# Kernel tuning notes

Measured on AMD Instinct MI355X. Metric: run time of the kernel, lower is better.

The kernel has to match this reference:

```python
import jax, jax.numpy as jnp
import numpy as np
import math

S, B, D, H = 2048, 4, 1024, 16
DH = D // H

def setup_inputs() -> dict:
    key = jax.random.key(0)
    ks = jax.random.split(key, 6)
    x = jax.random.normal(ks[0], (S, B, D), dtype=jnp.float32)
    # causal additive mask (finite large negative for numerical safety)
    i = jnp.arange(S)
    attn_mask = jnp.where(i[None, :] > i[:, None], jnp.float32(-1e9), jnp.float32(0.0))
    beta = jnp.zeros((H,), dtype=jnp.float32)  # per-head log-scale, init 0 -> exp=1
    xav = math.sqrt(6.0 / (D + D))  # xavier_uniform bound
    Wq = jax.random.uniform(ks[1], (D, D), minval=-xav, maxval=xav, dtype=jnp.float32)
    Wk = jax.random.uniform(ks[2], (D, D), minval=-xav, maxval=xav, dtype=jnp.float32)
    Wv = jax.random.uniform(ks[3], (D, D), minval=-xav, maxval=xav, dtype=jnp.float32)
    Wo = jax.random.uniform(ks[4], (D, D), minval=-xav, maxval=xav, dtype=jnp.float32)
    z = jnp.zeros((D,), dtype=jnp.float32)
    return {"x": x, "attn_mask": attn_mask, "beta": beta,
            "Wq": Wq, "bq": z, "Wk": Wk, "bk": z, "Wv": Wv, "bv": z, "Wo": Wo, "bo": z}

def reference(x, attn_mask, beta, Wq, bq, Wk, bk, Wv, bv, Wo, bo):
    s, b, d = x.shape
    h, dh = H, DH
    q = x @ Wq.T + bq  # (s, b, d)
    k = x @ Wk.T + bk
    v = x @ Wv.T + bv
    # attn_sink: append zero key/value token, pad mask with a zero column
    k = jnp.concatenate([k, jnp.zeros((1, b, d), k.dtype)], axis=0)  # (s+1, b, d)
    v = jnp.concatenate([v, jnp.zeros((1, b, d), v.dtype)], axis=0)
    mask = jnp.pad(attn_mask, ((0, 0), (0, 1)))  # (s, s+1)
    t = s + 1
    # split heads: (seq, b, h, dh) -> (b, h, seq, dh)
    qh = q.reshape(s, b, h, dh).transpose(1, 2, 0, 3)
    kh = k.reshape(t, b, h, dh).transpose(1, 2, 0, 3)
    vh = v.reshape(t, b, h, dh).transpose(1, 2, 0, 3)
    scale = (jnp.exp(beta) * math.sqrt(dh))[None, :, None, None]
    qh = qh / scale
    scores = jnp.einsum('bhsd,bhtd->bhst', qh, kh) + mask[None, None]
    w = jax.nn.softmax(scores, axis=-1)
    out = jnp.einsum('bhst,bhtd->bhsd', w, vh)  # (b, h, s, dh)
    out = out.transpose(2, 0, 1, 3).reshape(s, b, d)
    return out @ Wo.T + bo
```

## Files before the change

### kernel.cpp

```cpp
#include <hip/hip_runtime.h>
#include <hip/hip_bf16.h>
#include <math.h>

#define S_LEN   2048
#define BATCH   4
#define DMODEL  1024
#define NHEAD   16
#define DHEAD   64
#define MROWS   (S_LEN * BATCH)

typedef __bf16 bf16;
typedef __bf16 bf16x8 __attribute__((ext_vector_type(8)));
typedef __bf16 bf16x4 __attribute__((ext_vector_type(4)));
typedef short  short4_t __attribute__((ext_vector_type(4)));
typedef float  f32x4  __attribute__((ext_vector_type(4)));

#define LOG2E 1.4426950408889634f

#define AS1C(p) (const __attribute__((address_space(1))) void*)(p)
#define AS3(p)  (__attribute__((address_space(3))) void*)(p)


__global__ __launch_bounds__(256) void cast_bf16(const float* __restrict__ in,
                                                 bf16* __restrict__ out, int n8) {
    int i = blockIdx.x * 256 + threadIdx.x;
    if (i >= n8) return;
    const float4* p = (const float4*)in;
    float4 a = p[i * 2], b = p[i * 2 + 1];
    bf16x8 o;
    o[0] = (bf16)a.x; o[1] = (bf16)a.y; o[2] = (bf16)a.z; o[3] = (bf16)a.w;
    o[4] = (bf16)b.x; o[5] = (bf16)b.y; o[6] = (bf16)b.z; o[7] = (bf16)b.w;
    *(bf16x8*)(out + (size_t)i * 8) = o;
}

__global__ __launch_bounds__(256) void cast3_bf16(const float* __restrict__ w0,
                                                  const float* __restrict__ w1,
                                                  const float* __restrict__ w2,
                                                  bf16* __restrict__ out) {
    const int seg = blockIdx.y;
    const float* in = (seg == 0) ? w0 : (seg == 1) ? w1 : w2;
    int i = blockIdx.x * 256 + threadIdx.x;
    const float4* p = (const float4*)in;
    float4 a = p[i * 2], b = p[i * 2 + 1];
    bf16x8 o;
    o[0] = (bf16)a.x; o[1] = (bf16)a.y; o[2] = (bf16)a.z; o[3] = (bf16)a.w;
    o[4] = (bf16)b.x; o[5] = (bf16)b.y; o[6] = (bf16)b.z; o[7] = (bf16)b.w;
    *(bf16x8*)(out + (size_t)seg * DMODEL * DMODEL + (size_t)i * 8) = o;
}

#define GEMM_CORE(A_, W_, KDIM_)                                                        \
    constexpr int BK = 32;                                                              \
    __shared__ __align__(16) bf16 sA[128 * BK];                                         \
    __shared__ __align__(16) bf16 sB[128 * BK];                                         \
    const int t    = threadIdx.x;                                                       \
    const int lane = t & 63;                                                            \
    const int wave = t >> 6;                                                            \
    const int bm = blockIdx.y * 128;                                                    \
    const int wm = (wave & 1) * 64;                                                     \
    const int wn = (wave >> 1) * 64;                                                    \
    const int lq = lane & 15;                                                           \
    const int lg = lane >> 4;                                                           \
    const int grow = wave * 32 + (lane >> 2);                                           \
    const int gcol = (lane & 3) * 8;                                                    \
    const bf16* Ap = A_ + (size_t)(bm + grow) * KDIM_ + gcol;                           \
    const bf16* Wp = W_ + (size_t)(bn + grow) * KDIM_ + gcol;                           \
    bf16* la0 = &sA[(wave * 32) * BK];                                                  \
    bf16* lb0 = &sB[(wave * 32) * BK];                                                  \
    f32x4 acc[4][4] = {};                                                               \
    for (int k0 = 0; k0 < KDIM_; k0 += BK) {                                            \
        __syncthreads();                                                                \
        __builtin_amdgcn_global_load_lds(AS1C(Ap + k0),                      AS3(la0),           16, 0, 0); \
        __builtin_amdgcn_global_load_lds(AS1C(Ap + (size_t)16 * KDIM_ + k0), AS3(la0 + 16 * BK), 16, 0, 0); \
        __builtin_amdgcn_global_load_lds(AS1C(Wp + k0),                      AS3(lb0),           16, 0, 0); \
        __builtin_amdgcn_global_load_lds(AS1C(Wp + (size_t)16 * KDIM_ + k0), AS3(lb0 + 16 * BK), 16, 0, 0); \
        __syncthreads();                                                                \
        const int koff = lg * 8;                                                        \
        bf16x8 af[4], bfr[4];                                                           \
        _Pragma("unroll")                                                               \
        for (int mt = 0; mt < 4; mt++)                                                  \
            af[mt] = *(const bf16x8*)&sA[(wm + mt * 16 + lq) * BK + koff];              \
        _Pragma("unroll")                                                               \
        for (int nt = 0; nt < 4; nt++)                                                  \
            bfr[nt] = *(const bf16x8*)&sB[(wn + nt * 16 + lq) * BK + koff];             \
        _Pragma("unroll")                                                               \
        for (int mt = 0; mt < 4; mt++)                                                  \
            _Pragma("unroll")                                                           \
            for (int nt = 0; nt < 4; nt++)                                              \
                acc[mt][nt] = __builtin_amdgcn_mfma_f32_16x16x32_bf16(                  \
                    af[mt], bfr[nt], acc[mt][nt], 0, 0, 0);                             \
    }                                                                                   \
    const int cr = lg * 4;                                                              \
    const int cc = lq;

__global__ __launch_bounds__(256) void qkv_gemm(const bf16* __restrict__ A,
                                                const bf16* __restrict__ W,
                                                const float* __restrict__ bq,
                                                const float* __restrict__ bk,
                                                const float* __restrict__ bv,
                                                const float* __restrict__ beta,
                                                bf16* __restrict__ Qo,
                                                bf16* __restrict__ Kp,
                                                bf16* __restrict__ Vp) {
    const int bn = blockIdx.x * 128;
    GEMM_CORE(A, W, DMODEL)

    const int seg = blockIdx.x >> 3;
    const int bnl = (blockIdx.x & 7) * 128;
    const float* bias = (seg == 0) ? bq : (seg == 1) ? bk : bv;

    if (seg == 0) {
#pragma unroll
        for (int nt = 0; nt < 4; nt++) {
            const int col = bnl + wn + nt * 16 + cc;
            const float bvv = bias[col];
            const float sc = LOG2E / (__expf(beta[col >> 6]) * 8.0f);
#pragma unroll
            for (int mt = 0; mt < 4; mt++) {
                const int row = bm + wm + mt * 16 + cr;
#pragma unroll
                for (int r = 0; r < 4; r++) {
                    float v = (acc[mt][nt][r] + bvv) * sc;
                    Qo[(size_t)(row + r) * DMODEL + col] = (bf16)v;
                }
            }
        }
    } else {
        bf16* out = (seg == 1) ? Kp : Vp;
        const int h = (bnl + wn) >> 6;
#pragma unroll
        for (int mt = 0; mt < 4; mt++) {
            const int S0  = (bm + wm + mt * 16) >> 2;
            const int t16 = S0 >> 4;
            const int m4  = (S0 >> 2) & 3;
#pragma unroll
            for (int nt = 0; nt < 4; nt++) {
                const int col = bnl + wn + nt * 16 + cc;
                const float bvv = bias[col];
#pragma unroll
                for (int r = 0; r < 4; r++) {
                    float v = acc[mt][nt][r] + bvv;
                    size_t addr;
                    if (seg == 1) {
                        addr = ((size_t)((r * 16 + h) * 128 + t16)) * 1024
                             + (nt >> 1) * 512
                             + ((S0 & 15) + lg + 16 * ((nt & 1) * 2 + (lq >> 3))) * 8
                             + (lq & 7);
                    } else {
                        addr = ((size_t)((r * 16 + h) * 128 + t16)) * 1024
                             + nt * 256 + (lq + 16 * m4) * 4 + lg;
                    }
                    out[addr] = (bf16)v;
                }
            }
        }
    }
}

__global__ __launch_bounds__(256) void gemm_out(const bf16* __restrict__ A,
                                                const bf16* __restrict__ W,
                                                const float* __restrict__ bias,
                                                float* __restrict__ C) {
    const int bn = blockIdx.x * 128;
    GEMM_CORE(A, W, DMODEL)
#pragma unroll
    for (int nt = 0; nt < 4; nt++) {
        const int col = bn + wn + nt * 16 + cc;
        const float bvv = bias[col];
#pragma unroll
        for (int mt = 0; mt < 4; mt++) {
            const int row = bm + wm + mt * 16 + cr;
#pragma unroll
            for (int r = 0; r < 4; r++)
                C[(size_t)(row + r) * DMODEL + col] = acc[mt][nt][r] + bvv;
        }
    }
}

__global__ __launch_bounds__(256, 3) void attn_kernel(const bf16* __restrict__ Q,
                                                      const bf16* __restrict__ Kp,
                                                      const bf16* __restrict__ Vp,
                                                      bf16* __restrict__ O) {
    __shared__ __align__(16) float sO[64 * 65];
    __shared__ __align__(16) float sL[256];

    const int t    = threadIdx.x;
    const int lane = t & 63;
    const int wave = t >> 6;
    const int lq = lane & 15;
    const int lg = lane >> 4;
    const int qi = (int)gridDim.x - 1 - (int)blockIdx.x;
    const int h = blockIdx.y;
    const int b = blockIdx.z;
    const int qb = qi * 64;

    bf16x8 qf[4][2];
#pragma unroll
    for (int nt = 0; nt < 4; nt++)
#pragma unroll
        for (int kc = 0; kc < 2; kc++)
            qf[nt][kc] = *(const bf16x8*)
                &Q[((size_t)(qb + nt * 16 + lq) * BATCH + b) * DMODEL + h * DHEAD + kc * 32 + lg * 8];

    f32x4 o_acc[4][4] = {};
    float l_lane[4] = {0.f, 0.f, 0.f, 0.f};

    const bf16* Kb = Kp + (size_t)(b * NHEAD + h) * 131072;
    const bf16* Vb = Vp + (size_t)(b * NHEAD + h) * 131072;

    bf16x8 kc0 = *(const bf16x8*)(Kb + (size_t)wave * 1024 + lane * 8);
    bf16x8 kc1 = *(const bf16x8*)(Kb + (size_t)wave * 1024 + 512 + lane * 8);
    bf16x4 vc0 = *(const bf16x4*)(Vb + (size_t)wave * 1024 +   0 + lane * 4);
    bf16x4 vc1 = *(const bf16x4*)(Vb + (size_t)wave * 1024 + 256 + lane * 4);
    bf16x4 vc2 = *(const bf16x4*)(Vb + (size_t)wave * 1024 + 512 + lane * 4);
    bf16x4 vc3 = *(const bf16x4*)(Vb + (size_t)wave * 1024 + 768 + lane * 4);

    for (int kt = 0; kt <= qi; kt++) {
        const int tn = ((kt < qi) ? (kt + 1) : 0) * 4 + wave;
        const bf16* Kn = Kb + (size_t)tn * 1024;
        const bf16* Vn = Vb + (size_t)tn * 1024;
        bf16x8 kn0 = *(const bf16x8*)(Kn + lane * 8);
        bf16x8 kn1 = *(const bf16x8*)(Kn + 512 + lane * 8);
        bf16x4 vn0 = *(const bf16x4*)(Vn +   0 + lane * 4);
        bf16x4 vn1 = *(const bf16x4*)(Vn + 256 + lane * 4);
        bf16x4 vn2 = *(const bf16x4*)(Vn + 512 + lane * 4);
        bf16x4 vn3 = *(const bf16x4*)(Vn + 768 + lane * 4);

        f32x4 st[4];
#pragma unroll
        for (int nt = 0; nt < 4; nt++) {
            f32x4 a = {};
            a = __builtin_amdgcn_mfma_f32_16x16x32_bf16(kc0, qf[nt][0], a, 0, 0, 0);
            a = __builtin_amdgcn_mfma_f32_16x16x32_bf16(kc1, qf[nt][1], a, 0, 0, 0);
            st[nt] = a;
        }

        if (kt == qi) {
#pragma unroll
            for (int nt = 0; nt < 4; nt++)
#pragma unroll
                for (int r = 0; r < 4; r++)
                    if (wave * 16 + lg * 4 + r > nt * 16 + lq) st[nt][r] = -1e30f;
        }

        short4_t pf[4];
#pragma unroll
        for (int nt = 0; nt < 4; nt++) {
            float p0 = __builtin_amdgcn_exp2f(st[nt][0]);
            float p1 = __builtin_amdgcn_exp2f(st[nt][1]);
            float p2 = __builtin_amdgcn_exp2f(st[nt][2]);
            float p3 = __builtin_amdgcn_exp2f(st[nt][3]);
            l_lane[nt] += (p0 + p1) + (p2 + p3);
            bf16x4 pv;
            pv[0] = (bf16)p0; pv[1] = (bf16)p1; pv[2] = (bf16)p2; pv[3] = (bf16)p3;
            pf[nt] = __builtin_bit_cast(short4_t, pv);
        }

        short4_t va0 = __builtin_bit_cast(short4_t, vc0);
        short4_t va1 = __builtin_bit_cast(short4_t, vc1);
        short4_t va2 = __builtin_bit_cast(short4_t, vc2);
        short4_t va3 = __builtin_bit_cast(short4_t, vc3);
#pragma unroll
        for (int nt = 0; nt < 4; nt++) {
            o_acc[0][nt] = __builtin_amdgcn_mfma_f32_16x16x16bf16_1k(va0, pf[nt], o_acc[0][nt], 0, 0, 0);
            o_acc[1][nt] = __builtin_amdgcn_mfma_f32_16x16x16bf16_1k(va1, pf[nt], o_acc[1][nt], 0, 0, 0);
            o_acc[2][nt] = __builtin_amdgcn_mfma_f32_16x16x16bf16_1k(va2, pf[nt], o_acc[2][nt], 0, 0, 0);
            o_acc[3][nt] = __builtin_amdgcn_mfma_f32_16x16x16bf16_1k(va3, pf[nt], o_acc[3][nt], 0, 0, 0);
        }

        kc0 = kn0; kc1 = kn1;
        vc0 = vn0; vc1 = vn1; vc2 = vn2; vc3 = vn3;
    }

#pragma unroll
    for (int nt = 0; nt < 4; nt++) {
        float v = l_lane[nt];
        v += __shfl_xor(v, 16);
        v += __shfl_xor(v, 32);
        if (lg == 0) sL[wave * 64 + nt * 16 + lq] = v;
    }

#pragma unroll
    for (int rd = 0; rd < 4; rd++) {
#pragma unroll
        for (int dtc = 0; dtc < 4; dtc++) {
            if (((wave + rd) & 3) == dtc) {
                if (rd == 0) {
#pragma unroll
                    for (int nt = 0; nt < 4; nt++)
#pragma unroll
                        for (int r = 0; r < 4; r++)
                            sO[(dtc * 16 + lg * 4 + r) * 65 + nt * 16 + lq] = o_acc[dtc][nt][r];
                } else {
#pragma unroll
                    for (int nt = 0; nt < 4; nt++)
#pragma unroll
                        for (int r = 0; r < 4; r++)
                            sO[(dtc * 16 + lg * 4 + r) * 65 + nt * 16 + lq] += o_acc[dtc][nt][r];
                }
            }
        }
        __syncthreads();
    }

    const int dt = wave;
    float rec[4];
#pragma unroll
    for (int nt = 0; nt < 4; nt++) {
        float lt = 1.0f + sL[nt * 16 + lq] + sL[64 + nt * 16 + lq]
                 + sL[128 + nt * 16 + lq] + sL[192 + nt * 16 + lq];
        rec[nt] = 1.0f / lt;
    }
#pragma unroll
    for (int nt = 0; nt < 4; nt++) {
        bf16x4 ov;
#pragma unroll
        for (int r = 0; r < 4; r++)
            ov[r] = (bf16)(sO[(dt * 16 + lg * 4 + r) * 65 + nt * 16 + lq] * rec[nt]);
        *(bf16x4*)&O[((size_t)(qb + nt * 16 + lq) * BATCH + b) * DMODEL + h * DHEAD + dt * 16 + lg * 4] = ov;
    }
}

extern "C" void kernel_launch(void* const* d_in, const int* in_sizes, int n_in,
                              void* d_out, int out_size, void* d_ws, size_t ws_size,
                              hipStream_t stream) {
    const float* x    = (const float*)d_in[0];
    const float* beta = (const float*)d_in[2];
    const float* Wq   = (const float*)d_in[3];
    const float* bq   = (const float*)d_in[4];
    const float* Wk   = (const float*)d_in[5];
    const float* bk   = (const float*)d_in[6];
    const float* Wv   = (const float*)d_in[7];
    const float* bv   = (const float*)d_in[8];
    const float* Wo   = (const float*)d_in[9];
    const float* bo   = (const float*)d_in[10];
    float* out = (float*)d_out;

    char* ws = (char*)d_ws;
    size_t off = 0;
    auto alloc = [&](size_t bytes) -> void* {
        void* p = ws + off;
        off += (bytes + 255) & ~(size_t)255;
        return p;
    };
    const size_t xbytes = (size_t)MROWS * DMODEL * sizeof(bf16);
    const size_t wbytes = (size_t)DMODEL * DMODEL * sizeof(bf16);
    bf16* xb   = (bf16*)alloc(xbytes);
    bf16* wqkv = (bf16*)alloc(3 * wbytes);
    bf16* wob  = (bf16*)alloc(wbytes);
    bf16* qws  = (bf16*)alloc(xbytes);
    bf16* kpb  = (bf16*)alloc(xbytes);
    bf16* vpb  = (bf16*)alloc(xbytes);
    bf16* aob  = (bf16*)alloc(xbytes);

    const int nx8 = MROWS * DMODEL / 8;
    const int nw8 = DMODEL * DMODEL / 8;
    cast_bf16<<<(nx8 + 255) / 256, 256, 0, stream>>>(x, xb, nx8);
    cast_bf16<<<(nw8 + 255) / 256, 256, 0, stream>>>(Wo, wob, nw8);
    dim3 c3grid(nw8 / 256, 3);
    cast3_bf16<<<c3grid, 256, 0, stream>>>(Wq, Wk, Wv, wqkv);

    dim3 qgrid(3 * DMODEL / 128, MROWS / 128);
    qkv_gemm<<<qgrid, 256, 0, stream>>>(xb, wqkv, bq, bk, bv, beta, qws, kpb, vpb);

    dim3 agrid(S_LEN / 64, NHEAD, BATCH);
    attn_kernel<<<agrid, 256, 0, stream>>>(qws, kpb, vpb, aob);

    dim3 ogrid(DMODEL / 128, MROWS / 128);
    gemm_out<<<ogrid, 256, 0, stream>>>(aob, wob, bo, out);
}
```

Before: 308.7 us.

## Process two KV tiles per attention iteration with 8-wide V layout and merged weight casts

The attention loop is restructured to handle two 64-key tiles per iteration, prefetching both next tiles, with a diagonal-masked tail tile. The V projection layout written by the QKV GEMM is changed so each lane loads V with 16-byte bf16x8 loads instead of four 8-byte loads. Launch bounds drop from 3 to 2 waves per SIMD to allow the extra registers, and the Wo cast is folded into a single four-segment cast launch. The aim is more memory-level parallelism and fewer load instructions per tile, at the cost of higher register pressure and lower occupancy.

```diff
diff --git a/kernel.cpp b/kernel.cpp
--- a/kernel.cpp
+++ b/kernel.cpp
@@ -33,12 +33,13 @@
     *(bf16x8*)(out + (size_t)i * 8) = o;
 }
 
-__global__ __launch_bounds__(256) void cast3_bf16(const float* __restrict__ w0,
+__global__ __launch_bounds__(256) void cast4_bf16(const float* __restrict__ w0,
                                                   const float* __restrict__ w1,
                                                   const float* __restrict__ w2,
+                                                  const float* __restrict__ w3,
                                                   bf16* __restrict__ out) {
     const int seg = blockIdx.y;
-    const float* in = (seg == 0) ? w0 : (seg == 1) ? w1 : w2;
+    const float* in = (seg == 0) ? w0 : (seg == 1) ? w1 : (seg == 2) ? w2 : w3;
     int i = blockIdx.x * 256 + threadIdx.x;
     const float4* p = (const float4*)in;
     float4 a = p[i * 2], b = p[i * 2 + 1];
@@ -147,7 +148,8 @@
                              + (lq & 7);
                     } else {
                         addr = ((size_t)((r * 16 + h) * 128 + t16)) * 1024
-                             + nt * 256 + (lq + 16 * m4) * 4 + lg;
+                             + (nt >> 1) * 512 + (cc + 16 * m4) * 8
+                             + (nt & 1) * 4 + lg;
                     }
                     out[addr] = (bf16)v;
                 }
@@ -176,7 +178,53 @@
     }
 }
 
-__global__ __launch_bounds__(256, 3) void attn_kernel(const bf16* __restrict__ Q,
+#define ATTN_TILE(kc0_, kc1_, vv0_, vv1_, DIAG_)                                \
+    {                                                                           \
+        f32x4 st[4];                                                            \
+        _Pragma("unroll")                                                       \
+        for (int nt = 0; nt < 4; nt++) {                                        \
+            f32x4 a = {};                                                       \
+            a = __builtin_amdgcn_mfma_f32_16x16x32_bf16(kc0_, qf[nt][0], a, 0, 0, 0); \
+            a = __builtin_amdgcn_mfma_f32_16x16x32_bf16(kc1_, qf[nt][1], a, 0, 0, 0); \
+            st[nt] = a;                                                         \
+        }                                                                       \
+        if (DIAG_) {                                                            \
+            _Pragma("unroll")                                                   \
+            for (int nt = 0; nt < 4; nt++)                                      \
+                _Pragma("unroll")                                               \
+                for (int r = 0; r < 4; r++)                                     \
+                    if (wave * 16 + lg * 4 + r > nt * 16 + lq) st[nt][r] = -1e30f; \
+        }                                                                       \
+        short4_t pfr[4];                                                        \
+        _Pragma("unroll")                                                       \
+        for (int nt = 0; nt < 4; nt++) {                                        \
+            float p0 = __builtin_amdgcn_exp2f(st[nt][0]);                       \
+            float p1 = __builtin_amdgcn_exp2f(st[nt][1]);                       \
+            float p2 = __builtin_amdgcn_exp2f(st[nt][2]);                       \
+            float p3 = __builtin_amdgcn_exp2f(st[nt][3]);                       \
+            l_lane[nt] += (p0 + p1) + (p2 + p3);                                \
+            bf16x4 pv;                                                          \
+            pv[0] = (bf16)p0; pv[1] = (bf16)p1; pv[2] = (bf16)p2; pv[3] = (bf16)p3; \
+            pfr[nt] = __builtin_bit_cast(short4_t, pv);                         \
+        }                                                                       \
+        bf16x4 w0 = __builtin_shufflevector(vv0_, vv0_, 0, 1, 2, 3);            \
+        bf16x4 w1 = __builtin_shufflevector(vv0_, vv0_, 4, 5, 6, 7);            \
+        bf16x4 w2 = __builtin_shufflevector(vv1_, vv1_, 0, 1, 2, 3);            \
+        bf16x4 w3 = __builtin_shufflevector(vv1_, vv1_, 4, 5, 6, 7);            \
+        short4_t va0 = __builtin_bit_cast(short4_t, w0);                        \
+        short4_t va1 = __builtin_bit_cast(short4_t, w1);                        \
+        short4_t va2 = __builtin_bit_cast(short4_t, w2);                        \
+        short4_t va3 = __builtin_bit_cast(short4_t, w3);                        \
+        _Pragma("unroll")                                                       \
+        for (int nt = 0; nt < 4; nt++) {                                        \
+            o_acc[0][nt] = __builtin_amdgcn_mfma_f32_16x16x16bf16_1k(va0, pfr[nt], o_acc[0][nt], 0, 0, 0); \
+            o_acc[1][nt] = __builtin_amdgcn_mfma_f32_16x16x16bf16_1k(va1, pfr[nt], o_acc[1][nt], 0, 0, 0); \
+            o_acc[2][nt] = __builtin_amdgcn_mfma_f32_16x16x16bf16_1k(va2, pfr[nt], o_acc[2][nt], 0, 0, 0); \
+            o_acc[3][nt] = __builtin_amdgcn_mfma_f32_16x16x16bf16_1k(va3, pfr[nt], o_acc[3][nt], 0, 0, 0); \
+        }                                                                       \
+    }
+
+__global__ __launch_bounds__(256, 2) void attn_kernel(const bf16* __restrict__ Q,
                                                       const bf16* __restrict__ Kp,
                                                       const bf16* __restrict__ Vp,
                                                       bf16* __restrict__ O) {
@@ -207,68 +255,43 @@
     const bf16* Kb = Kp + (size_t)(b * NHEAD + h) * 131072;
     const bf16* Vb = Vp + (size_t)(b * NHEAD + h) * 131072;
 
-    bf16x8 kc0 = *(const bf16x8*)(Kb + (size_t)wave * 1024 + lane * 8);
-    bf16x8 kc1 = *(const bf16x8*)(Kb + (size_t)wave * 1024 + 512 + lane * 8);
-    bf16x4 vc0 = *(const bf16x4*)(Vb + (size_t)wave * 1024 +   0 + lane * 4);
-    bf16x4 vc1 = *(const bf16x4*)(Vb + (size_t)wave * 1024 + 256 + lane * 4);
-    bf16x4 vc2 = *(const bf16x4*)(Vb + (size_t)wave * 1024 + 512 + lane * 4);
-    bf16x4 vc3 = *(const bf16x4*)(Vb + (size_t)wave * 1024 + 768 + lane * 4);
-
-    for (int kt = 0; kt <= qi; kt++) {
-        const int tn = ((kt < qi) ? (kt + 1) : 0) * 4 + wave;
-        const bf16* Kn = Kb + (size_t)tn * 1024;
-        const bf16* Vn = Vb + (size_t)tn * 1024;
-        bf16x8 kn0 = *(const bf16x8*)(Kn + lane * 8);
-        bf16x8 kn1 = *(const bf16x8*)(Kn + 512 + lane * 8);
-        bf16x4 vn0 = *(const bf16x4*)(Vn +   0 + lane * 4);
-        bf16x4 vn1 = *(const bf16x4*)(Vn + 256 + lane * 4);
-        bf16x4 vn2 = *(const bf16x4*)(Vn + 512 + lane * 4);
-        bf16x4 vn3 = *(const bf16x4*)(Vn + 768 + lane * 4);
-
-        f32x4 st[4];
-#pragma unroll
-        for (int nt = 0; nt < 4; nt++) {
-            f32x4 a = {};
-            a = __builtin_amdgcn_mfma_f32_16x16x32_bf16(kc0, qf[nt][0], a, 0, 0, 0);
-            a = __builtin_amdgcn_mfma_f32_16x16x32_bf16(kc1, qf[nt][1], a, 0, 0, 0);
-            st[nt] = a;
-        }
-
-        if (kt == qi) {
-#pragma unroll
-            for (int nt = 0; nt < 4; nt++)
-#pragma unroll
-                for (int r = 0; r < 4; r++)
-                    if (wave * 16 + lg * 4 + r > nt * 16 + lq) st[nt][r] = -1e30f;
-        }
-
-        short4_t pf[4];
-#pragma unroll
-        for (int nt = 0; nt < 4; nt++) {
-            float p0 = __builtin_amdgcn_exp2f(st[nt][0]);
-            float p1 = __builtin_amdgcn_exp2f(st[nt][1]);
-            float p2 = __builtin_amdgcn_exp2f(st[nt][2]);
-            float p3 = __builtin_amdgcn_exp2f(st[nt][3]);
-            l_lane[nt] += (p0 + p1) + (p2 + p3);
-            bf16x4 pv;
-            pv[0] = (bf16)p0; pv[1] = (bf16)p1; pv[2] = (bf16)p2; pv[3] = (bf16)p3;
-            pf[nt] = __builtin_bit_cast(short4_t, pv);
-        }
-
-        short4_t va0 = __builtin_bit_cast(short4_t, vc0);
-        short4_t va1 = __builtin_bit_cast(short4_t, vc1);
-        short4_t va2 = __builtin_bit_cast(short4_t, vc2);
-        short4_t va3 = __builtin_bit_cast(short4_t, vc3);
-#pragma unroll
-        for (int nt = 0; nt < 4; nt++) {
-            o_acc[0][nt] = __builtin_amdgcn_mfma_f32_16x16x16bf16_1k(va0, pf[nt], o_acc[0][nt], 0, 0, 0);
-            o_acc[1][nt] = __builtin_amdgcn_mfma_f32_16x16x16bf16_1k(va1, pf[nt], o_acc[1][nt], 0, 0, 0);
-            o_acc[2][nt] = __builtin_amdgcn_mfma_f32_16x16x16bf16_1k(va2, pf[nt], o_acc[2][nt], 0, 0, 0);
-            o_acc[3][nt] = __builtin_amdgcn_mfma_f32_16x16x16bf16_1k(va3, pf[nt], o_acc[3][nt], 0, 0, 0);
-        }
-
-        kc0 = kn0; kc1 = kn1;
-        vc0 = vn0; vc1 = vn1; vc2 = vn2; vc3 = vn3;
+    const bf16* kpA = Kb + wave * 1024 + lane * 8;
+    const bf16* kpB = kpA + 4096;
+    const bf16* vpA = Vb + wave * 1024 + lane * 8;
+    const bf16* vpB = vpA + 4096;
+
+    bf16x8 kA0 = *(const bf16x8*)kpA;
+    bf16x8 kA1 = *(const bf16x8*)(kpA + 512);
+    bf16x8 vA0 = *(const bf16x8*)vpA;
+    bf16x8 vA1 = *(const bf16x8*)(vpA + 512);
+    bf16x8 kB0 = *(const bf16x8*)kpB;
+    bf16x8 kB1 = *(const bf16x8*)(kpB + 512);
+    bf16x8 vB0 = *(const bf16x8*)vpB;
+    bf16x8 vB1 = *(const bf16x8*)(vpB + 512);
+
+    const int pairs = (qi + 1) >> 1;
+    const int tail  = (qi + 1) & 1;
+
+    for (int i = 0; i < pairs; i++) {
+        kpA += 8192; kpB += 8192; vpA += 8192; vpB += 8192;
+        bf16x8 nkA0 = *(const bf16x8*)kpA;
+        bf16x8 nkA1 = *(const bf16x8*)(kpA + 512);
+        bf16x8 nvA0 = *(const bf16x8*)vpA;
+        bf16x8 nvA1 = *(const bf16x8*)(vpA + 512);
+        bf16x8 nkB0 = *(const bf16x8*)kpB;
+        bf16x8 nkB1 = *(const bf16x8*)(kpB + 512);
+        bf16x8 nvB0 = *(const bf16x8*)vpB;
+        bf16x8 nvB1 = *(const bf16x8*)(vpB + 512);
+
+        ATTN_TILE(kA0, kA1, vA0, vA1, false)
+        const bool diagB = (2 * i + 1 == qi);
+        ATTN_TILE(kB0, kB1, vB0, vB1, diagB)
+
+        kA0 = nkA0; kA1 = nkA1; vA0 = nvA0; vA1 = nvA1;
+        kB0 = nkB0; kB1 = nkB1; vB0 = nvB0; vB1 = nvB1;
+    }
+    if (tail) {
+        ATTN_TILE(kA0, kA1, vA0, vA1, true)
     }
 
 #pragma unroll
@@ -345,19 +368,19 @@
     const size_t xbytes = (size_t)MROWS * DMODEL * sizeof(bf16);
     const size_t wbytes = (size_t)DMODEL * DMODEL * sizeof(bf16);
     bf16* xb   = (bf16*)alloc(xbytes);
-    bf16* wqkv = (bf16*)alloc(3 * wbytes);
-    bf16* wob  = (bf16*)alloc(wbytes);
+    bf16* wall = (bf16*)alloc(4 * wbytes);
     bf16* qws  = (bf16*)alloc(xbytes);
     bf16* kpb  = (bf16*)alloc(xbytes);
     bf16* vpb  = (bf16*)alloc(xbytes);
     bf16* aob  = (bf16*)alloc(xbytes);
+    bf16* wqkv = wall;
+    bf16* wob  = wall + (size_t)3 * DMODEL * DMODEL;
 
     const int nx8 = MROWS * DMODEL / 8;
     const int nw8 = DMODEL * DMODEL / 8;
     cast_bf16<<<(nx8 + 255) / 256, 256, 0, stream>>>(x, xb, nx8);
-    cast_bf16<<<(nw8 + 255) / 256, 256, 0, stream>>>(Wo, wob, nw8);
-    dim3 c3grid(nw8 / 256, 3);
-    cast3_bf16<<<c3grid, 256, 0, stream>>>(Wq, Wk, Wv, wqkv);
+    dim3 c4grid(nw8 / 256, 4);
+    cast4_bf16<<<c4grid, 256, 0, stream>>>(Wq, Wk, Wv, Wo, wall);
 
     dim3 qgrid(3 * DMODEL / 128, MROWS / 128);
     qkv_gemm<<<qgrid, 256, 0, stream>>>(xb, wqkv, bq, bk, bv, beta, qws, kpb, vpb);
```

After: 312.3 us. Within noise of the previous version (+1.2%).
